# Optimization experiments

Hardware: AMD Instinct MI355X
Metric: run time of the kernel (lower is better)

The kernel has to match this reference:

```python
import jax, jax.numpy as jnp
import numpy as np

N_NODES = 100000
N_FEAT = 512
HIDDEN = 64
N_CLASSES = 40
N_EDGES = 3200000
K = 10
ALPHA = 0.1


def setup_inputs() -> dict:
    key = jax.random.key(0)
    k1, k2, k3, k4 = jax.random.split(key, 4)
    x = jax.random.normal(k1, (N_NODES, N_FEAT), dtype=jnp.float32)
    # Glorot-ish scaled linear weights
    W1 = jax.random.normal(k2, (N_FEAT, HIDDEN), dtype=jnp.float32) / np.sqrt(N_FEAT)
    b1 = jnp.zeros((HIDDEN,), dtype=jnp.float32)
    W2 = jax.random.normal(k3, (HIDDEN, N_CLASSES), dtype=jnp.float32) / np.sqrt(HIDDEN)
    b2 = jnp.zeros((N_CLASSES,), dtype=jnp.float32)
    edge_index = jax.random.randint(k4, (2, N_EDGES), 0, N_NODES, dtype=jnp.int64)
    return {"x": x, "W1": W1, "b1": b1, "W2": W2, "b2": b2, "edge_index": edge_index}


def reference(x, W1, b1, W2, b2, edge_index):
    n = x.shape[0]
    # MLP (dropout is identity in eval mode)
    h = jnp.maximum(x @ W1 + b1, 0.0)
    h = h @ W2 + b2  # [N, C]

    # gcn_norm with self-loops: A_hat = D^{-1/2} (A + I) D^{-1/2}
    loops = jnp.arange(n, dtype=edge_index.dtype)
    row = jnp.concatenate([edge_index[0], loops])  # source (gather)
    col = jnp.concatenate([edge_index[1], loops])  # target (scatter)
    deg = jax.ops.segment_sum(jnp.ones(row.shape, dtype=h.dtype), col, num_segments=n)
    dinv = jnp.where(deg > 0, jax.lax.rsqrt(deg), 0.0)
    norm = dinv[row] * dinv[col]  # [E + N]

    h0 = h

    def step(z, _):
        msg = norm[:, None] * z[row]                      # gather + scale
        agg = jax.ops.segment_sum(msg, col, num_segments=n)  # scatter-add
        z = ALPHA * h0 + (1.0 - ALPHA) * agg
        return z, None

    z, _ = jax.lax.scan(step, h0, None, length=K)
    return jax.nn.log_softmax(z, axis=1)
```

## Files before the change

### kernel.cpp

```cpp
#include <hip/hip_runtime.h>
#include <hip/hip_bf16.h>
#include <hip/hip_fp16.h>

#define N_NODES   100000
#define N_FEAT    512
#define HIDDEN    64
#define N_CLASSES 40
#define KITER     10
#define ALPHA     0.1f
#define ZP        64
#define HPITCH    72
#define NXCD      8
#define WIN       (N_NODES / NXCD)
#define SUBCAP    65536
#define PARTB     2048
#define CAP       384

typedef __attribute__((ext_vector_type(8))) short bf16x8;
typedef __attribute__((ext_vector_type(4))) float f32x4;

__device__ __forceinline__ float bf2f(unsigned short u) {
    union { unsigned int i; float f; } c;
    c.i = ((unsigned int)u) << 16;
    return c.f;
}
__device__ __forceinline__ unsigned short f2bf(float f) {
    union { float f; unsigned int u; } c; c.f = f;
    unsigned int r = c.u + 0x7FFFu + ((c.u >> 16) & 1u);
    return (unsigned short)(r >> 16);
}

__global__ void zero_cur_kernel(int* __restrict__ cur, int* __restrict__ flags) {
    int t = threadIdx.x;
    if (t < 65) cur[t] = 0;
    if (t >= 65 && t < 67) flags[t - 65] = 0;
}

__global__ void detect_float_kernel(const unsigned short* __restrict__ w1raw,
                                    int* __restrict__ flags) {
    int i = blockIdx.x * blockDim.x + threadIdx.x;
    if (i < 32768) {
        unsigned short u = w1raw[i];
        if ((u & 0x7F80u) == 0x7F80u) atomicAdd(&flags[0], 1);
    }
}

__global__ void detect_edge_kernel(const int* __restrict__ ei, int* __restrict__ flags) {
    int i = blockIdx.x * blockDim.x + threadIdx.x;
    if (i < 2048) {
        if (ei[2 * i + 1] != 0) atomicAdd(&flags[1], 1);
    }
}

__global__ void pack_w1_kernel(const void* __restrict__ W1p, const int* __restrict__ flags,
                               unsigned short* __restrict__ pb) {
    int idx = blockIdx.x * 256 + threadIdx.x;
    int j    = idx & 7;
    int lane = (idx >> 3) & 63;
    int ktnt = idx >> 9;
    int kt = ktnt & 15, nt = ktnt >> 4;
    int k = kt * 32 + (lane >> 4) * 8 + j;
    int n = nt * 16 + (lane & 15);
    unsigned short v;
    if (flags[0] > 0) v = f2bf(((const float*)W1p)[k * HIDDEN + n]);
    else              v = ((const unsigned short*)W1p)[k * HIDDEN + n];
    pb[idx] = v;
}

__global__ void pack_w2_kernel(const void* __restrict__ W2p, const int* __restrict__ flags,
                               unsigned short* __restrict__ pb2) {
    int idx = blockIdx.x * 256 + threadIdx.x;
    if (idx >= 3072) return;
    int j    = idx & 7;
    int lane = (idx >> 3) & 63;
    int ktnt = idx >> 9;
    int kt = ktnt & 1, nt = ktnt >> 1;
    int k = kt * 32 + (lane >> 4) * 8 + j;
    int n = nt * 16 + (lane & 15);
    unsigned short v = 0;
    if (n < N_CLASSES) {
        if (flags[0] > 0) v = f2bf(((const float*)W2p)[k * N_CLASSES + n]);
        else              v = ((const unsigned short*)W2p)[k * N_CLASSES + n];
    }
    pb2[idx] = v;
}

__global__ __launch_bounds__(256) void mlp_kernel(
    const void* __restrict__ xp,
    const unsigned short* __restrict__ pb,
    const unsigned short* __restrict__ pb2,
    const void* __restrict__ b1p,
    const void* __restrict__ b2p,
    const int* __restrict__ flags,
    const float* __restrict__ dinv,
    float* __restrict__ h0,
    __half* __restrict__ zh0)
{
    __shared__ unsigned short hsb[16 * HPITCH];
    const int t    = threadIdx.x;
    const int wave = t >> 6;
    const int lane = t & 63;
    const int quad = lane >> 4;
    const int ml   = lane & 15;
    const int base = blockIdx.x * 16;
    const int isf32 = flags[0] > 0;

    const bf16x8* pbv = (const bf16x8*)pb;

    f32x4 acc = {0.f, 0.f, 0.f, 0.f};
    if (!isf32) {
        const unsigned short* xrow = (const unsigned short*)xp
                                   + (size_t)(base + ml) * N_FEAT + quad * 8;
        #pragma unroll
        for (int kt = 0; kt < 16; ++kt) {
            bf16x8 a = *(const bf16x8*)(xrow + kt * 32);
            bf16x8 b = pbv[(wave * 16 + kt) * 64 + lane];
            acc = __builtin_amdgcn_mfma_f32_16x16x32_bf16(a, b, acc, 0, 0, 0);
        }
    } else {
        const float* xf = (const float*)xp + (size_t)(base + ml) * N_FEAT + quad * 8;
        #pragma unroll
        for (int kt = 0; kt < 16; ++kt) {
            float4 lo = *(const float4*)(xf + kt * 32);
            float4 hi = *(const float4*)(xf + kt * 32 + 4);
            bf16x8 a;
            a[0] = (short)f2bf(lo.x); a[1] = (short)f2bf(lo.y);
            a[2] = (short)f2bf(lo.z); a[3] = (short)f2bf(lo.w);
            a[4] = (short)f2bf(hi.x); a[5] = (short)f2bf(hi.y);
            a[6] = (short)f2bf(hi.z); a[7] = (short)f2bf(hi.w);
            bf16x8 b = pbv[(wave * 16 + kt) * 64 + lane];
            acc = __builtin_amdgcn_mfma_f32_16x16x32_bf16(a, b, acc, 0, 0, 0);
        }
    }

    float b1v = isf32 ? ((const float*)b1p)[wave * 16 + ml]
                      : bf2f(((const unsigned short*)b1p)[wave * 16 + ml]);
    #pragma unroll
    for (int r = 0; r < 4; ++r)
        hsb[(quad * 4 + r) * HPITCH + wave * 16 + ml] = f2bf(fmaxf(acc[r] + b1v, 0.0f));
    __syncthreads();

    if (wave < 3) {
        const bf16x8* pb2v = (const bf16x8*)pb2;
        f32x4 acc2 = {0.f, 0.f, 0.f, 0.f};
        #pragma unroll
        for (int kt = 0; kt < 2; ++kt) {
            bf16x8 a = *(const bf16x8*)(hsb + ml * HPITCH + kt * 32 + quad * 8);
            bf16x8 b = pb2v[(wave * 2 + kt) * 64 + lane];
            acc2 = __builtin_amdgcn_mfma_f32_16x16x32_bf16(a, b, acc2, 0, 0, 0);
        }
        int n = wave * 16 + ml;
        if (n < N_CLASSES) {
            float b2v = isf32 ? ((const float*)b2p)[n] : bf2f(((const unsigned short*)b2p)[n]);
            #pragma unroll
            for (int r = 0; r < 4; ++r) {
                int node = base + quad * 4 + r;
                float v = acc2[r] + b2v;
                h0[(size_t)node * N_CLASSES + n] = v;
                zh0[(size_t)node * ZP + n] = __float2half(v * dinv[node]);
            }
        }
    }
}

__global__ void zero_pad_kernel(__half* __restrict__ a, __half* __restrict__ b) {
    int t = threadIdx.x;
    if (t < ZP)            a[(size_t)N_NODES * ZP + t]        = __float2half(0.0f);
    else if (t < 2 * ZP)   b[(size_t)N_NODES * ZP + (t - ZP)] = __float2half(0.0f);
}

__global__ __launch_bounds__(256) void partition_kernel(
    const int* __restrict__ ei, const int* __restrict__ flags,
    unsigned int* __restrict__ sub,
    int* __restrict__ cur, int2* __restrict__ ovf, int E)
{
    __shared__ unsigned buf[NXCD][CAP];
    __shared__ int cnt_lds[NXCD];
    __shared__ unsigned base_s[NXCD];

    const int i64f = flags[1] == 0;
    const int xcd  = blockIdx.x & 7;
    const int per  = (E + PARTB - 1) / PARTB;
    const int e0   = blockIdx.x * per;
    const int e1   = min(e0 + per, E);

    if (threadIdx.x < NXCD) cnt_lds[threadIdx.x] = 0;
    __syncthreads();

    for (int e = e0 + threadIdx.x; e < e1; e += 256) {
        int c = i64f ? __builtin_nontemporal_load(ei + 2 * E + 2 * e)
                     : __builtin_nontemporal_load(ei + E + e);
        int r = i64f ? __builtin_nontemporal_load(ei + 2 * e)
                     : __builtin_nontemporal_load(ei + e);
        int w = c / WIN;
        unsigned pk = (unsigned)r | ((unsigned)(c - w * WIN) << 17);
        int slot = atomicAdd(&cnt_lds[w], 1);
        if (slot < CAP) buf[w][slot] = pk;
        else { int op = atomicAdd(cur + 64, 1); ovf[op] = make_int2(r, c); }
    }
    __syncthreads();

    const int g   = threadIdx.x >> 5;
    const int l32 = threadIdx.x & 31;
    const int n   = min(cnt_lds[g], CAP);
    if (l32 == 0 && n > 0) base_s[g] = (unsigned)atomicAdd(&cur[g * 8 + xcd], n);
    __syncthreads();
    if (n > 0) {
        unsigned base = base_s[g];
        unsigned bslot = (unsigned)(g * 8 + xcd) * SUBCAP;
        for (int i = l32; i < n; i += 32) {
            unsigned p = base + (unsigned)i;
            unsigned pk = buf[g][i];
            if (p < SUBCAP) sub[bslot + p] = pk;
            else {
                int op = atomicAdd(cur + 64, 1);
                ovf[op] = make_int2((int)(pk & 0x1FFFFu), g * WIN + (int)(pk >> 17));
            }
        }
    }
}

__global__ __launch_bounds__(1024) void hist_kernel(
    const unsigned int* __restrict__ sub, const int* __restrict__ cur,
    const int2* __restrict__ ovf, int* __restrict__ hists)
{
    __shared__ int h[WIN];
    const int w = blockIdx.x & 7;
    const int s = blockIdx.x >> 3;
    for (int off = threadIdx.x; off < WIN; off += 1024) h[off] = 0;
    __syncthreads();
    int n = min(cur[w * 8 + s], SUBCAP);
    const unsigned int* sp = sub + (size_t)(w * 8 + s) * SUBCAP;
    for (int i = threadIdx.x; i < n; i += 1024)
        atomicAdd(&h[sp[i] >> 17], 1);
    if (s == 7) {
        int ov = cur[64];
        for (int i = threadIdx.x; i < ov; i += 1024) {
            int2 rc = ovf[i];
            int ww = rc.y / WIN;
            if (ww == w) atomicAdd(&h[rc.y - ww * WIN], 1);
        }
    }
    __syncthreads();
    for (int off = threadIdx.x; off < WIN; off += 1024)
        hists[(size_t)(w * 8 + s) * WIN + off] = h[off];
}

__global__ void cnt_kernel(const int* __restrict__ hists, int* __restrict__ cnt,
                           float* __restrict__ dinv) {
    int i = blockIdx.x * 256 + threadIdx.x;
    if (i >= N_NODES) return;
    int w = i / WIN, off = i - w * WIN;
    int c = 0;
    #pragma unroll
    for (int x = 0; x < 8; ++x) c += hists[(size_t)(w * 8 + x) * WIN + off];
    cnt[i] = c;
    dinv[i] = rsqrtf((float)c + 1.0f);
}

__global__ __launch_bounds__(1024) void scan_kernel(
    const int* __restrict__ cnt, int* __restrict__ rptr, int E)
{
    __shared__ int wsum[16];
    __shared__ int carry_s, tiletot_s;
    const int t = threadIdx.x, wave = t >> 6, lane = t & 63;
    if (t == 0) carry_s = 0;
    __syncthreads();
    for (int base = 0; base < N_NODES; base += 4096) {
        int i0 = base + t * 4;
        int v0 = (i0 + 0 < N_NODES) ? cnt[i0 + 0] : 0;
        int v1 = (i0 + 1 < N_NODES) ? cnt[i0 + 1] : 0;
        int v2 = (i0 + 2 < N_NODES) ? cnt[i0 + 2] : 0;
        int v3 = (i0 + 3 < N_NODES) ? cnt[i0 + 3] : 0;
        int tl = v0 + v1 + v2 + v3;
        int sc = tl;
        #pragma unroll
        for (int off = 1; off < 64; off <<= 1) {
            int u = __shfl_up(sc, off, 64);
            if (lane >= off) sc += u;
        }
        if (lane == 63) wsum[wave] = sc;
        int wexcl = sc - tl;
        __syncthreads();
        if (wave == 0) {
            int wv = (lane < 16) ? wsum[lane] : 0;
            int ws = wv;
            #pragma unroll
            for (int off = 1; off < 16; off <<= 1) {
                int u = __shfl_up(ws, off, 64);
                if (lane >= off) ws += u;
            }
            if (lane < 16) wsum[lane] = ws - wv;
            if (lane == 15) tiletot_s = ws;
        }
        __syncthreads();
        int P  = carry_s + wsum[wave] + wexcl;
        if (i0 + 0 < N_NODES) rptr[i0 + 0] = P;
        if (i0 + 1 < N_NODES) rptr[i0 + 1] = P + v0;
        if (i0 + 2 < N_NODES) rptr[i0 + 2] = P + v0 + v1;
        if (i0 + 3 < N_NODES) rptr[i0 + 3] = P + v0 + v1 + v2;
        __syncthreads();
        if (t == 0) carry_s += tiletot_s;
        __syncthreads();
    }
    if (t == 0) rptr[N_NODES] = E;
}

__global__ __launch_bounds__(1024) void scatter_kernel(
    const unsigned int* __restrict__ sub, const int* __restrict__ cur,
    const int* __restrict__ hists, const int2* __restrict__ ovf,
    const int* __restrict__ rptr, int* __restrict__ srcidx)
{
    __shared__ int curs[WIN];
    const int w = blockIdx.x & 7;
    const int s = blockIdx.x >> 3;
    for (int off = threadIdx.x; off < WIN; off += 1024) {
        int base = rptr[w * WIN + off];
        for (int x = 0; x < s; ++x)
            base += hists[(size_t)(w * 8 + x) * WIN + off];
        curs[off] = base;
    }
    __syncthreads();
    int n = min(cur[w * 8 + s], SUBCAP);
    const unsigned int* sp = sub + (size_t)(w * 8 + s) * SUBCAP;
    for (int i = threadIdx.x; i < n; i += 1024) {
        unsigned pk = sp[i];
        int slot = atomicAdd(&curs[pk >> 17], 1);
        srcidx[slot] = (int)(pk & 0x1FFFFu);
    }
    if (s == 7) {
        int ov = cur[64];
        for (int i = threadIdx.x; i < ov; i += 1024) {
            int2 rc = ovf[i];
            int ww = rc.y / WIN;
            if (ww == w) {
                int slot = atomicAdd(&curs[rc.y - ww * WIN], 1);
                srcidx[slot] = rc.x;
            }
        }
    }
}

__global__ __launch_bounds__(256) void prop_kernel(
    const __half* __restrict__ zh, const float* __restrict__ h0,
    const float* __restrict__ dinv, const int* __restrict__ rptr,
    const int* __restrict__ srcidx, __half* __restrict__ zout)
{
    const int wave = threadIdx.x >> 6;
    const int lane = threadIdx.x & 63;
    const int g    = lane >> 4;
    const int l    = lane & 15;
    const int node = blockIdx.x * 16 + wave * 4 + g;
    const int c0   = l * 4;

    const int beg = rptr[node];
    const int end = rptr[node + 1];
    int nch = (end - beg + 15) >> 4;
    int m1    = max(nch, __shfl_xor(nch, 16, 64));
    int maxch = max(m1,  __shfl_xor(m1, 32, 64));

    float di = dinv[node];
    uint2 yself = *(const uint2*)(zh + ((size_t)node << 6) + c0);
    float h00 = 0.f, h01 = 0.f, h02 = 0.f, h03 = 0.f;
    if (c0 < N_CLASSES) {
        const float* hp = h0 + (size_t)node * N_CLASSES + c0;
        h00 = hp[0]; h01 = hp[1]; h02 = hp[2]; h03 = hp[3];
    }

    float a0 = 0.f, a1 = 0.f, a2 = 0.f, a3 = 0.f;
    float b0 = 0.f, b1 = 0.f, b2 = 0.f, b3 = 0.f;

    for (int ch = 0; ch < maxch; ++ch) {
        int idx = beg + ch * 16 + l;
        int sw  = (idx < end) ? srcidx[idx] : N_NODES;

        #pragma unroll
        for (int i = 0; i < 16; i += 2) {
            int s0 = __shfl(sw, (g << 4) + i,     64);
            int s1 = __shfl(sw, (g << 4) + i + 1, 64);
            uint2 z0 = *(const uint2*)(zh + ((size_t)s0 << 6) + c0);
            uint2 z1 = *(const uint2*)(zh + ((size_t)s1 << 6) + c0);
            const __half2* p0 = (const __half2*)&z0;
            const __half2* p1 = (const __half2*)&z1;
            float2 f00 = __half22float2(p0[0]);
            float2 f01 = __half22float2(p0[1]);
            float2 f10 = __half22float2(p1[0]);
            float2 f11 = __half22float2(p1[1]);
            a0 += f00.x; a1 += f00.y; a2 += f01.x; a3 += f01.y;
            b0 += f10.x; b1 += f10.y; b2 += f11.x; b3 += f11.y;
        }
    }

    if (c0 < N_CLASSES) {
        const __half2* ps = (const __half2*)&yself;
        float2 s01 = __half22float2(ps[0]);
        float2 s23 = __half22float2(ps[1]);
        float kk = (1.0f - ALPHA) * di;
        float o0 = ALPHA * h00 + kk * (a0 + b0 + s01.x);
        float o1 = ALPHA * h01 + kk * (a1 + b1 + s01.y);
        float o2 = ALPHA * h02 + kk * (a2 + b2 + s23.x);
        float o3 = ALPHA * h03 + kk * (a3 + b3 + s23.y);
        __half2 q01 = __floats2half2_rn(di * o0, di * o1);
        __half2 q23 = __floats2half2_rn(di * o2, di * o3);
        uint2 st;
        st.x = *(unsigned int*)&q01;
        st.y = *(unsigned int*)&q23;
        *(uint2*)(zout + ((size_t)node << 6) + c0) = st;
    }
}

__global__ __launch_bounds__(256) void lsm_kernel(
    const __half* __restrict__ zh, const float* __restrict__ dinv,
    const int* __restrict__ flags, void* __restrict__ outp)
{
    const int wave = threadIdx.x >> 6;
    const int lane = threadIdx.x & 63;
    const int node = blockIdx.x * 4 + wave;
    const int isf32 = flags[0] > 0;

    float di = dinv[node];
    float v = (lane < N_CLASSES)
            ? __half2float(zh[(size_t)node * ZP + lane]) / di : -1e30f;
    float m = v;
    #pragma unroll
    for (int o = 32; o; o >>= 1) m = fmaxf(m, __shfl_xor(m, o, 64));
    float e = (lane < N_CLASSES) ? expf(v - m) : 0.0f;
    float s = e;
    #pragma unroll
    for (int o = 32; o; o >>= 1) s += __shfl_xor(s, o, 64);
    float ls = logf(s);
    if (lane < N_CLASSES) {
        float r = v - m - ls;
        size_t idx = (size_t)node * N_CLASSES + lane;
        if (isf32) ((float*)outp)[idx] = r;
        else       ((__hip_bfloat16*)outp)[idx] = __float2bfloat16(r);
    }
}

extern "C" void kernel_launch(void* const* d_in, const int* in_sizes, int n_in,
                              void* d_out, int out_size, void* d_ws, size_t ws_size,
                              hipStream_t stream)
{
    const void* x  = d_in[0];
    const void* W1 = d_in[1];
    const void* b1 = d_in[2];
    const void* W2 = d_in[3];
    const void* b2 = d_in[4];
    const int* ei = (const int*)d_in[5];
    const int E = in_sizes[5] / 2;

    char* ws = (char*)d_ws;
    size_t off = 0;
    auto carve = [&](size_t bytes) -> void* {
        void* p = ws + off;
        off = (off + bytes + 255) & ~(size_t)255;
        return p;
    };
    float*  h0    = (float*) carve((size_t)N_NODES * N_CLASSES * 4);
    __half* zhA   = (__half*)carve((size_t)(N_NODES + 1) * ZP * 2);
    __half* zhB   = (__half*)carve((size_t)(N_NODES + 1) * ZP * 2);
    int*    cnt   = (int*)   carve((size_t)N_NODES * 4);
    float*  dinv  = (float*) carve((size_t)N_NODES * 4);
    int*    rptr  = (int*)   carve((size_t)(N_NODES + 1) * 4);
    int*    srcidx= (int*)   carve((size_t)E * 4);
    unsigned int* sub = (unsigned int*)carve((size_t)64 * SUBCAP * 4);
    int*    hists = (int*)   carve((size_t)64 * WIN * 4);
    int*    cur   = (int*)   carve(65 * sizeof(int));
    unsigned short* pb  = (unsigned short*)carve(32768 * 2);
    unsigned short* pb2 = (unsigned short*)carve(3072 * 2);
    int*    flags = (int*)   carve(2 * sizeof(int));
    (void)ws_size; (void)n_in; (void)out_size;

    int2* ovf = (int2*)zhA;

    const int nodeBlocks = N_NODES / 4;
    const int mlpBlocks  = N_NODES / 16;
    const int propBlocks = N_NODES / 16;
    const int cntBlocks  = (N_NODES + 255) / 256;

    zero_cur_kernel<<<1, 128, 0, stream>>>(cur, flags);
    detect_float_kernel<<<128, 256, 0, stream>>>((const unsigned short*)W1, flags);
    detect_edge_kernel<<<8, 256, 0, stream>>>(ei, flags);
    pack_w1_kernel<<<128, 256, 0, stream>>>(W1, flags, pb);
    pack_w2_kernel<<<12, 256, 0, stream>>>(W2, flags, pb2);

    partition_kernel<<<PARTB, 256, 0, stream>>>(ei, flags, sub, cur, ovf, E);
    hist_kernel<<<64, 1024, 0, stream>>>(sub, cur, ovf, hists);
    cnt_kernel<<<cntBlocks, 256, 0, stream>>>(hists, cnt, dinv);
    scan_kernel<<<1, 1024, 0, stream>>>(cnt, rptr, E);
    scatter_kernel<<<64, 1024, 0, stream>>>(sub, cur, hists, ovf, rptr, srcidx);
    zero_pad_kernel<<<1, 128, 0, stream>>>(zhA, zhB);

    mlp_kernel<<<mlpBlocks, 256, 0, stream>>>(x, pb, pb2, b1, b2, flags, dinv, h0, zhA);

    const __half* zin = zhA;
    __half* zout = zhB;
    const __half* zlast = zhA;
    for (int it = 0; it < KITER; ++it) {
        prop_kernel<<<propBlocks, 256, 0, stream>>>(zin, h0, dinv, rptr, srcidx, zout);
        zlast = zout;
        zin = zout;
        zout = (zout == zhB) ? zhA : zhB;
    }

    lsm_kernel<<<nodeBlocks, 256, 0, stream>>>(zlast, dinv, flags, d_out);
}
```

Baseline: 1.074 ms.

## Retile MLP per-wave, bucket edges by source window, prefetch neighbor indices

```diff
diff --git a/kernel.cpp b/kernel.cpp
--- a/kernel.cpp
+++ b/kernel.cpp
@@ -14,7 +14,7 @@
 #define WIN       (N_NODES / NXCD)
 #define SUBCAP    65536
 #define PARTB     2048
-#define CAP       384
+#define CAP       96
 
 typedef __attribute__((ext_vector_type(8))) short bf16x8;
 typedef __attribute__((ext_vector_type(4))) float f32x4;
@@ -96,68 +96,89 @@
     float* __restrict__ h0,
     __half* __restrict__ zh0)
 {
-    __shared__ unsigned short hsb[16 * HPITCH];
+    __shared__ unsigned short hsb[4][16 * HPITCH];
     const int t    = threadIdx.x;
     const int wave = t >> 6;
     const int lane = t & 63;
     const int quad = lane >> 4;
     const int ml   = lane & 15;
-    const int base = blockIdx.x * 16;
+    const int mbase = blockIdx.x * 64 + wave * 16;
     const int isf32 = flags[0] > 0;
+    const bool valid = mbase < N_NODES;
 
     const bf16x8* pbv = (const bf16x8*)pb;
-
-    f32x4 acc = {0.f, 0.f, 0.f, 0.f};
-    if (!isf32) {
-        const unsigned short* xrow = (const unsigned short*)xp
-                                   + (size_t)(base + ml) * N_FEAT + quad * 8;
+    f32x4 acc[4];
+    #pragma unroll
+    for (int nt = 0; nt < 4; ++nt) acc[nt] = (f32x4){0.f, 0.f, 0.f, 0.f};
+
+    if (valid) {
+        if (!isf32) {
+            const unsigned short* xrow = (const unsigned short*)xp
+                                       + (size_t)(mbase + ml) * N_FEAT + quad * 8;
+            #pragma unroll
+            for (int kt = 0; kt < 16; ++kt) {
+                bf16x8 a = *(const bf16x8*)(xrow + kt * 32);
+                #pragma unroll
+                for (int nt = 0; nt < 4; ++nt)
+                    acc[nt] = __builtin_amdgcn_mfma_f32_16x16x32_bf16(
+                        a, pbv[(nt * 16 + kt) * 64 + lane], acc[nt], 0, 0, 0);
+            }
+        } else {
+            const float* xf = (const float*)xp + (size_t)(mbase + ml) * N_FEAT + quad * 8;
+            #pragma unroll
+            for (int kt = 0; kt < 16; ++kt) {
+                float4 lo = *(const float4*)(xf + kt * 32);
+                float4 hi = *(const float4*)(xf + kt * 32 + 4);
+                bf16x8 a;
+                a[0] = (short)f2bf(lo.x); a[1] = (short)f2bf(lo.y);
+                a[2] = (short)f2bf(lo.z); a[3] = (short)f2bf(lo.w);
+                a[4] = (short)f2bf(hi.x); a[5] = (short)f2bf(hi.y);
+                a[6] = (short)f2bf(hi.z); a[7] = (short)f2bf(hi.w);
+                #pragma unroll
+                for (int nt = 0; nt < 4; ++nt)
+                    acc[nt] = __builtin_amdgcn_mfma_f32_16x16x32_bf16(
+                        a, pbv[(nt * 16 + kt) * 64 + lane], acc[nt], 0, 0, 0);
+            }
+        }
+
         #pragma unroll
-        for (int kt = 0; kt < 16; ++kt) {
-            bf16x8 a = *(const bf16x8*)(xrow + kt * 32);
-            bf16x8 b = pbv[(wave * 16 + kt) * 64 + lane];
-            acc = __builtin_amdgcn_mfma_f32_16x16x32_bf16(a, b, acc, 0, 0, 0);
-        }
-    } else {
-        const float* xf = (const float*)xp + (size_t)(base + ml) * N_FEAT + quad * 8;
+        for (int nt = 0; nt < 4; ++nt) {
+            float b1v = isf32 ? ((const float*)b1p)[nt * 16 + ml]
+                              : bf2f(((const unsigned short*)b1p)[nt * 16 + ml]);
+            #pragma unroll
+            for (int r = 0; r < 4; ++r)
+                hsb[wave][(quad * 4 + r) * HPITCH + nt * 16 + ml] =
+                    f2bf(fmaxf(acc[nt][r] + b1v, 0.0f));
+        }
+    }
+    __syncthreads();
+
+    if (valid) {
+        const bf16x8* pb2v = (const bf16x8*)pb2;
+        f32x4 acc2[3];
         #pragma unroll
-        for (int kt = 0; kt < 16; ++kt) {
-            float4 lo = *(const float4*)(xf + kt * 32);
-            float4 hi = *(const float4*)(xf + kt * 32 + 4);
-            bf16x8 a;
-            a[0] = (short)f2bf(lo.x); a[1] = (short)f2bf(lo.y);
-            a[2] = (short)f2bf(lo.z); a[3] = (short)f2bf(lo.w);
-            a[4] = (short)f2bf(hi.x); a[5] = (short)f2bf(hi.y);
-            a[6] = (short)f2bf(hi.z); a[7] = (short)f2bf(hi.w);
-            bf16x8 b = pbv[(wave * 16 + kt) * 64 + lane];
-            acc = __builtin_amdgcn_mfma_f32_16x16x32_bf16(a, b, acc, 0, 0, 0);
-        }
-    }
-
-    float b1v = isf32 ? ((const float*)b1p)[wave * 16 + ml]
-                      : bf2f(((const unsigned short*)b1p)[wave * 16 + ml]);
-    #pragma unroll
-    for (int r = 0; r < 4; ++r)
-        hsb[(quad * 4 + r) * HPITCH + wave * 16 + ml] = f2bf(fmaxf(acc[r] + b1v, 0.0f));
-    __syncthreads();
-
-    if (wave < 3) {
-        const bf16x8* pb2v = (const bf16x8*)pb2;
-        f32x4 acc2 = {0.f, 0.f, 0.f, 0.f};
+        for (int n2 = 0; n2 < 3; ++n2) acc2[n2] = (f32x4){0.f, 0.f, 0.f, 0.f};
         #pragma unroll
         for (int kt = 0; kt < 2; ++kt) {
-            bf16x8 a = *(const bf16x8*)(hsb + ml * HPITCH + kt * 32 + quad * 8);
-            bf16x8 b = pb2v[(wave * 2 + kt) * 64 + lane];
-            acc2 = __builtin_amdgcn_mfma_f32_16x16x32_bf16(a, b, acc2, 0, 0, 0);
-        }
-        int n = wave * 16 + ml;
-        if (n < N_CLASSES) {
-            float b2v = isf32 ? ((const float*)b2p)[n] : bf2f(((const unsigned short*)b2p)[n]);
+            bf16x8 a = *(const bf16x8*)(&hsb[wave][ml * HPITCH + kt * 32 + quad * 8]);
             #pragma unroll
-            for (int r = 0; r < 4; ++r) {
-                int node = base + quad * 4 + r;
-                float v = acc2[r] + b2v;
-                h0[(size_t)node * N_CLASSES + n] = v;
-                zh0[(size_t)node * ZP + n] = __float2half(v * dinv[node]);
+            for (int n2 = 0; n2 < 3; ++n2)
+                acc2[n2] = __builtin_amdgcn_mfma_f32_16x16x32_bf16(
+                    a, pb2v[(n2 * 2 + kt) * 64 + lane], acc2[n2], 0, 0, 0);
+        }
+        #pragma unroll
+        for (int n2 = 0; n2 < 3; ++n2) {
+            int n = n2 * 16 + ml;
+            if (n < N_CLASSES) {
+                float b2v = isf32 ? ((const float*)b2p)[n]
+                                  : bf2f(((const unsigned short*)b2p)[n]);
+                #pragma unroll
+                for (int r = 0; r < 4; ++r) {
+                    int node = mbase + quad * 4 + r;
+                    float v = acc2[n2][r] + b2v;
+                    h0[(size_t)node * N_CLASSES + n] = v;
+                    zh0[(size_t)node * ZP + n] = __float2half(v * dinv[node]);
+                }
             }
         }
     }
@@ -174,17 +195,16 @@
     unsigned int* __restrict__ sub,
     int* __restrict__ cur, int2* __restrict__ ovf, int E)
 {
-    __shared__ unsigned buf[NXCD][CAP];
-    __shared__ int cnt_lds[NXCD];
-    __shared__ unsigned base_s[NXCD];
+    __shared__ unsigned buf[64][CAP];
+    __shared__ int cnt_lds[64];
+    __shared__ unsigned base_s[64];
 
     const int i64f = flags[1] == 0;
-    const int xcd  = blockIdx.x & 7;
     const int per  = (E + PARTB - 1) / PARTB;
     const int e0   = blockIdx.x * per;
     const int e1   = min(e0 + per, E);
 
-    if (threadIdx.x < NXCD) cnt_lds[threadIdx.x] = 0;
+    if (threadIdx.x < 64) cnt_lds[threadIdx.x] = 0;
     __syncthreads();
 
     for (int e = e0 + threadIdx.x; e < e1; e += 256) {
@@ -192,29 +212,32 @@
                      : __builtin_nontemporal_load(ei + E + e);
         int r = i64f ? __builtin_nontemporal_load(ei + 2 * e)
                      : __builtin_nontemporal_load(ei + e);
-        int w = c / WIN;
-        unsigned pk = (unsigned)r | ((unsigned)(c - w * WIN) << 17);
-        int slot = atomicAdd(&cnt_lds[w], 1);
-        if (slot < CAP) buf[w][slot] = pk;
+        int wd = c / WIN;
+        int ws = r / WIN;
+        int b  = wd * 8 + ws;
+        unsigned pk = (unsigned)r | ((unsigned)(c - wd * WIN) << 17);
+        int slot = atomicAdd(&cnt_lds[b], 1);
+        if (slot < CAP) buf[b][slot] = pk;
         else { int op = atomicAdd(cur + 64, 1); ovf[op] = make_int2(r, c); }
     }
     __syncthreads();
 
-    const int g   = threadIdx.x >> 5;
-    const int l32 = threadIdx.x & 31;
-    const int n   = min(cnt_lds[g], CAP);
-    if (l32 == 0 && n > 0) base_s[g] = (unsigned)atomicAdd(&cur[g * 8 + xcd], n);
+    const int g  = threadIdx.x >> 2;
+    const int l4 = threadIdx.x & 3;
+    const int n  = min(cnt_lds[g], CAP);
+    if (l4 == 0 && n > 0) base_s[g] = (unsigned)atomicAdd(&cur[g], n);
     __syncthreads();
     if (n > 0) {
         unsigned base = base_s[g];
-        unsigned bslot = (unsigned)(g * 8 + xcd) * SUBCAP;
-        for (int i = l32; i < n; i += 32) {
+        unsigned bslot = (unsigned)g * SUBCAP;
+        for (int i = l4; i < n; i += 4) {
             unsigned p = base + (unsigned)i;
             unsigned pk = buf[g][i];
             if (p < SUBCAP) sub[bslot + p] = pk;
             else {
                 int op = atomicAdd(cur + 64, 1);
-                ovf[op] = make_int2((int)(pk & 0x1FFFFu), g * WIN + (int)(pk >> 17));
+                ovf[op] = make_int2((int)(pk & 0x1FFFFu),
+                                    (g >> 3) * WIN + (int)(pk >> 17));
             }
         }
     }
@@ -370,9 +393,12 @@
     float a0 = 0.f, a1 = 0.f, a2 = 0.f, a3 = 0.f;
     float b0 = 0.f, b1 = 0.f, b2 = 0.f, b3 = 0.f;
 
+    int idx0 = beg + l;
+    int sw = (idx0 < end) ? srcidx[idx0] : N_NODES;
+
     for (int ch = 0; ch < maxch; ++ch) {
-        int idx = beg + ch * 16 + l;
-        int sw  = (idx < end) ? srcidx[idx] : N_NODES;
+        int idxn = beg + (ch + 1) * 16 + l;
+        int swn = (ch + 1 < maxch) ? ((idxn < end) ? srcidx[idxn] : N_NODES) : N_NODES;
 
         #pragma unroll
         for (int i = 0; i < 16; i += 2) {
@@ -389,6 +415,7 @@
             a0 += f00.x; a1 += f00.y; a2 += f01.x; a3 += f01.y;
             b0 += f10.x; b1 += f10.y; b2 += f11.x; b3 += f11.y;
         }
+        sw = swn;
     }
 
     if (c0 < N_CLASSES) {
@@ -474,7 +501,7 @@
     int2* ovf = (int2*)zhA;
 
     const int nodeBlocks = N_NODES / 4;
-    const int mlpBlocks  = N_NODES / 16;
+    const int mlpBlocks  = (N_NODES + 63) / 64;
     const int propBlocks = N_NODES / 16;
     const int cntBlocks  = (N_NODES + 255) / 256;
 
```

Measured after the change: 1.027 ms. -4.4%, faster.
